# Kernel optimization log

Hardware: AMD Instinct MI355X
Metric: run time of the kernel (lower is better)

## Reference

```python
import jax, jax.numpy as jnp
import numpy as np

MUL = 16          # multiplicity of every irrep block
N = 131072        # number of nodes

# orthonormal traceless-symmetric 3x3 basis, divided by sqrt(5).
_s = 1.0 / np.sqrt(2.0)
_M = np.zeros((5, 3, 3), dtype=np.float32)
_M[0, 0, 1] = _M[0, 1, 0] = _s
_M[1, 0, 2] = _M[1, 2, 0] = _s
_M[2, 1, 2] = _M[2, 2, 1] = _s
_M[3, 0, 0] = _s; _M[3, 1, 1] = -_s
_M[4] = np.diag([-1.0, -1.0, 2.0]).astype(np.float32) / np.sqrt(6.0)
C112 = jnp.asarray(np.transpose(_M, (1, 2, 0)) / np.sqrt(5.0))  # (3,3,5)

# e3nn TensorProduct normalization: irrep_normalization='component'
# (alpha = 2l_out+1), path_normalization='element' (divide by sum of
# mul_u*mul_v over paths into the same output irrep). 0e output receives
# two paths -> 2*MUL^2; 1o and 2e each receive one path -> MUL^2.
A000 = float(np.sqrt(1.0 / (2.0 * MUL * MUL)))                    # 0e x 0e -> 0e (w3j = 1)
A110 = float(np.sqrt(1.0 / (2.0 * MUL * MUL)) / np.sqrt(3.0))     # 1o x 1o -> 0e (w3j = d_ij/sqrt(3))
A101 = float(np.sqrt(3.0 / (MUL * MUL)) / np.sqrt(3.0))           # 1o x 0e -> 1o (w3j = d_ik/sqrt(3))
A112 = float(np.sqrt(5.0 / (MUL * MUL)))                          # 1o x 1o -> 2e


def setup_inputs() -> dict:
    key = jax.random.key(0)
    ks = jax.random.split(key, 6)
    f = lambda k, s: jax.random.normal(k, s, dtype=jnp.float32)
    return {
        "node_feats": f(ks[0], (N, 4 * MUL)),
        "node_messages": f(ks[1], (N, 4 * MUL)),
        "w000": f(ks[2], (MUL, MUL, MUL)),
        "w101": f(ks[3], (MUL, MUL, MUL)),
        "w110": f(ks[4], (MUL, MUL, MUL)),
        "w112": f(ks[5], (MUL, MUL, MUL)),
    }


def _tensor_square(x, w000, w101, w110, w112):
    """e3nn o3.TensorSquare('16x0e+16x1o', '16x0e+16x1o+16x2e') with 'uvw' weighted paths."""
    n = x.shape[0]
    x0 = x[:, :MUL]                          # (n, u)     l=0 block
    x1 = x[:, MUL:].reshape(n, MUL, 3)       # (n, u, i)  l=1 block (mul-major)

    # --- 0e output ---
    out0 = A000 * jnp.einsum('uvw,nu,nv->nw', w000, x0, x0)
    out0 = out0 + A110 * jnp.einsum('uvw,nui,nvi->nw', w110, x1, x1)

    # --- 1o output ---
    out1 = A101 * jnp.einsum('uvw,nuk,nv->nwk', w101, x1, x0)

    # --- 2e output (staged to keep intermediates small) ---
    t1 = jnp.einsum('nvj,ijk->nvik', x1, C112)        # (n, v, i, 5)
    t = jnp.einsum('nui,nvik->nuvk', x1, t1)          # (n, u, v, 5)
    out2 = A112 * jnp.einsum('uvw,nuvk->nwk', w112, t)

    return jnp.concatenate(
        [out0, out1.reshape(n, 3 * MUL), out2.reshape(n, 5 * MUL)], axis=1
    )  # (n, 144)


def reference(node_feats, node_messages, w000, w101, w110, w112):
    # SimpleNodeBlock: sum all nodewise tensors, then tensor square.
    return _tensor_square(node_feats + node_messages, w000, w101, w110, w112)
```

## Files before the change

### kernel.cpp

```cpp
#include <hip/hip_runtime.h>

#define MUL 16
#define NPAIR 136
#define NTILE 25

typedef __bf16 bf16x8 __attribute__((ext_vector_type(8)));
typedef float  f32x4  __attribute__((ext_vector_type(4)));

__device__ __forceinline__ void uv_of(int p, int& u, int& v) {
    if (p >= NPAIR) { u = 0; v = 0; return; }
    int uu = 0, rem = p;
    while (rem >= MUL - uu) { rem -= MUL - uu; ++uu; }
    u = uu; v = uu + rem;
}

__global__ void prep_weights(const float* __restrict__ w000,
                             const float* __restrict__ w101,
                             const float* __restrict__ w110,
                             const float* __restrict__ w112,
                             __bf16* __restrict__ wt) {
    const int gid = blockIdx.x * 256 + threadIdx.x;
    if (gid >= NTILE * 64) return;
    const int T = gid >> 6, lane = gid & 63;
    const int q = lane >> 4, w = lane & 15;

    const float A000   = 0.044194173824159216f;
    const float A110   = 0.025515518153991442f;
    const float A101   = 0.0625f;
    const float A112C1 = 0.044194173824159216f;

    bf16x8 frag = {};
    if (T < 10) {
        const int c = T >> 1, b = T & 1;
#pragma unroll
        for (int i = 0; i < 4; ++i) {
            const int p = 32 * c + 8 * q + 4 * b + i;
            if (p < NPAIR) {
                int u, v; uv_of(p, u, v);
                const int uvw = (u * MUL + v) * MUL + w;
                const int vuw = (v * MUL + u) * MUL + w;
                float f000, f110;
                if (u == v) { f000 = A000 * w000[uvw]; f110 = A110 * w110[uvw]; }
                else        { f000 = A000 * (w000[uvw] + w000[vuw]);
                              f110 = A110 * (w110[uvw] + w110[vuw]); }
                frag[2 * i]     = (__bf16)f000;
                frag[2 * i + 1] = (__bf16)f110;
            }
        }
    } else if (T < 20) {
        const int c = (T - 10) >> 1, b = (T - 10) & 1;
#pragma unroll
        for (int i = 0; i < 4; ++i) {
            const int p = 32 * c + 8 * q + 4 * b + i;
            if (p < NPAIR) {
                int u, v; uv_of(p, u, v);
                const int uvw = (u * MUL + v) * MUL + w;
                const int vuw = (v * MUL + u) * MUL + w;
                frag[2 * i]     = (__bf16)(A101 * w101[uvw]);
                frag[2 * i + 1] = (__bf16)((u == v) ? 0.f : A101 * w101[vuw]);
            }
        }
    } else {
        const int c = T - 20;
#pragma unroll
        for (int e = 0; e < 8; ++e) {
            const int p = 32 * c + 8 * q + e;
            if (p < NPAIR) {
                int u, v; uv_of(p, u, v);
                const int uvw = (u * MUL + v) * MUL + w;
                const int vuw = (v * MUL + u) * MUL + w;
                const float f112 = (u == v) ? A112C1 * w112[uvw]
                                            : A112C1 * (w112[uvw] + w112[vuw]);
                frag[e] = (__bf16)f112;
            }
        }
    }
    ((bf16x8*)wt)[T * 64 + lane] = frag;
}

#define SQ3f  1.7320508075688772f
#define ISQ3f 0.5773502691896258f

template<int E>
__device__ __forceinline__ void pair_feats(int d, const float* __restrict__ xrow,
        bf16x8& fS, bf16x8& f0, bf16x8& f1, bf16x8& f2,
        bf16x8& t0, bf16x8& t1, bf16x8& t2, bf16x8& t3, bf16x8& t4) {
    constexpr int sh = (E & 1) * 16;
    const int u = (d >> sh) & 0xff;
    const int v = (d >> (sh + 8)) & 0xff;
    const float4 xu = *(const float4*)(xrow + 4 * u);
    const float4 xv = *(const float4*)(xrow + 4 * v);
    const float o00 = xu.y * xv.y, o01 = xu.y * xv.z, o02 = xu.y * xv.w;
    const float o10 = xu.z * xv.y, o11 = xu.z * xv.z, o12 = xu.z * xv.w;
    const float o20 = xu.w * xv.y, o21 = xu.w * xv.z, o22 = xu.w * xv.w;
    const float s1 = (o00 + o11) + o22;
    constexpr int s2 = (E & 3) * 2;
    fS[s2]     = (__bf16)(xu.x * xv.x);
    fS[s2 + 1] = (__bf16)s1;
    f0[s2]     = (__bf16)(xu.y * xv.x);  f0[s2 + 1] = (__bf16)(xv.y * xu.x);
    f1[s2]     = (__bf16)(xu.z * xv.x);  f1[s2 + 1] = (__bf16)(xv.z * xu.x);
    f2[s2]     = (__bf16)(xu.w * xv.x);  f2[s2 + 1] = (__bf16)(xv.w * xu.x);
    t0[E] = (__bf16)(o01 + o10);
    t1[E] = (__bf16)(o02 + o20);
    t2[E] = (__bf16)(o12 + o21);
    t3[E] = (__bf16)(o00 - o11);
    t4[E] = (__bf16)(SQ3f * o22 - ISQ3f * s1);
}

__launch_bounds__(256, 3)
__global__ void tsq_kernel(const float* __restrict__ feats,
                           const float* __restrict__ msgs,
                           const __bf16* __restrict__ wtiles,
                           float* __restrict__ out) {
    __shared__ __align__(16) float xq[64 * 68];
    __shared__ __align__(16) int   uvt[80];

    const int tid = threadIdx.x;
    const long long blockNode = (long long)blockIdx.x * 64;

    if (tid < 80) {
        int u0, v0, u1, v1;
        uv_of(2 * tid,     u0, v0);
        uv_of(2 * tid + 1, u1, v1);
        uvt[tid] = u0 | (v0 << 8) | (u1 << 16) | (v1 << 24);
    }

    {
        const float4* f4p = (const float4*)(feats + blockNode * 64);
        const float4* m4p = (const float4*)(msgs  + blockNode * 64);
#pragma unroll
        for (int r = 0; r < 4; ++r) {
            const int li = r * 256 + tid;
            const int nd = li >> 4, f4 = li & 15;
            const float4 a = f4p[li];
            const float4 b = m4p[li];
            const float vals[4] = {a.x + b.x, a.y + b.y, a.z + b.z, a.w + b.w};
#pragma unroll
            for (int jj = 0; jj < 4; ++jj) {
                const int f = 4 * f4 + jj;
                int dst;
                if (f < 16) dst = nd * 68 + 4 * f;
                else {
                    const int g = f - 16;
                    const int v3 = (g * 171) >> 9;
                    dst = nd * 68 + 4 * v3 + 1 + (g - 3 * v3);
                }
                xq[dst] = vals[jj];
            }
        }
    }
    __syncthreads();

    const int lane = tid & 63;
    const int wid  = tid >> 6;
    const int m = lane & 15, q = lane >> 4;
    const float* xrow = xq + (wid * 16 + m) * 68;
    const bf16x8* wb = (const bf16x8*)wtiles;

    f32x4 accS  = {0.f, 0.f, 0.f, 0.f};
    f32x4 accP0 = {0.f, 0.f, 0.f, 0.f};
    f32x4 accP1 = {0.f, 0.f, 0.f, 0.f};
    f32x4 accP2 = {0.f, 0.f, 0.f, 0.f};
    f32x4 accT0 = {0.f, 0.f, 0.f, 0.f};
    f32x4 accT1 = {0.f, 0.f, 0.f, 0.f};
    f32x4 accT2 = {0.f, 0.f, 0.f, 0.f};
    f32x4 accT3 = {0.f, 0.f, 0.f, 0.f};
    f32x4 accT4 = {0.f, 0.f, 0.f, 0.f};

#pragma unroll
    for (int c = 0; c < 5; ++c) {
        const int4 uvd = *(const int4*)((const char*)uvt + 64 * c + 16 * q);
        bf16x8 t0 = {}, t1 = {}, t2 = {}, t3 = {}, t4 = {};
        {
            const bf16x8 bS = wb[(2 * c) * 64 + lane];
            const bf16x8 bP = wb[(10 + 2 * c) * 64 + lane];
            bf16x8 fS, f0, f1, f2;
            pair_feats<0>(uvd.x, xrow, fS, f0, f1, f2, t0, t1, t2, t3, t4);
            pair_feats<1>(uvd.x, xrow, fS, f0, f1, f2, t0, t1, t2, t3, t4);
            pair_feats<2>(uvd.y, xrow, fS, f0, f1, f2, t0, t1, t2, t3, t4);
            pair_feats<3>(uvd.y, xrow, fS, f0, f1, f2, t0, t1, t2, t3, t4);
            accS  = __builtin_amdgcn_mfma_f32_16x16x32_bf16(fS, bS, accS,  0, 0, 0);
            accP0 = __builtin_amdgcn_mfma_f32_16x16x32_bf16(f0, bP, accP0, 0, 0, 0);
            accP1 = __builtin_amdgcn_mfma_f32_16x16x32_bf16(f1, bP, accP1, 0, 0, 0);
            accP2 = __builtin_amdgcn_mfma_f32_16x16x32_bf16(f2, bP, accP2, 0, 0, 0);
        }
        {
            const bf16x8 bS = wb[(2 * c + 1) * 64 + lane];
            const bf16x8 bP = wb[(11 + 2 * c) * 64 + lane];
            bf16x8 fS, f0, f1, f2;
            pair_feats<4>(uvd.z, xrow, fS, f0, f1, f2, t0, t1, t2, t3, t4);
            pair_feats<5>(uvd.z, xrow, fS, f0, f1, f2, t0, t1, t2, t3, t4);
            pair_feats<6>(uvd.w, xrow, fS, f0, f1, f2, t0, t1, t2, t3, t4);
            pair_feats<7>(uvd.w, xrow, fS, f0, f1, f2, t0, t1, t2, t3, t4);
            accS  = __builtin_amdgcn_mfma_f32_16x16x32_bf16(fS, bS, accS,  0, 0, 0);
            accP0 = __builtin_amdgcn_mfma_f32_16x16x32_bf16(f0, bP, accP0, 0, 0, 0);
            accP1 = __builtin_amdgcn_mfma_f32_16x16x32_bf16(f1, bP, accP1, 0, 0, 0);
            accP2 = __builtin_amdgcn_mfma_f32_16x16x32_bf16(f2, bP, accP2, 0, 0, 0);
        }
        const bf16x8 bT = wb[(20 + c) * 64 + lane];
        accT0 = __builtin_amdgcn_mfma_f32_16x16x32_bf16(t0, bT, accT0, 0, 0, 0);
        accT1 = __builtin_amdgcn_mfma_f32_16x16x32_bf16(t1, bT, accT1, 0, 0, 0);
        accT2 = __builtin_amdgcn_mfma_f32_16x16x32_bf16(t2, bT, accT2, 0, 0, 0);
        accT3 = __builtin_amdgcn_mfma_f32_16x16x32_bf16(t3, bT, accT3, 0, 0, 0);
        accT4 = __builtin_amdgcn_mfma_f32_16x16x32_bf16(t4, bT, accT4, 0, 0, 0);
    }

#pragma unroll
    for (int r = 0; r < 4; ++r) {
        float* ob = out + (blockNode + wid * 16 + q * 4 + r) * 144;
        ob[m]              = accS[r];
        ob[16 + 3 * m + 0] = accP0[r];
        ob[16 + 3 * m + 1] = accP1[r];
        ob[16 + 3 * m + 2] = accP2[r];
        ob[64 + 5 * m + 0] = accT0[r];
        ob[64 + 5 * m + 1] = accT1[r];
        ob[64 + 5 * m + 2] = accT2[r];
        ob[64 + 5 * m + 3] = accT3[r];
        ob[64 + 5 * m + 4] = accT4[r];
    }
}

extern "C" void kernel_launch(void* const* d_in, const int* in_sizes, int n_in,
                              void* d_out, int out_size, void* d_ws, size_t ws_size,
                              hipStream_t stream) {
    const float* feats = (const float*)d_in[0];
    const float* msgs  = (const float*)d_in[1];
    const float* w000  = (const float*)d_in[2];
    const float* w101  = (const float*)d_in[3];
    const float* w110  = (const float*)d_in[4];
    const float* w112  = (const float*)d_in[5];
    __bf16* wt = (__bf16*)d_ws;
    float* out = (float*)d_out;

    const int n = in_sizes[0] / (4 * MUL);

    prep_weights<<<(NTILE * 64 + 255) / 256, 256, 0, stream>>>(w000, w101, w110, w112, wt);
    tsq_kernel<<<n / 64, 256, 0, stream>>>(feats, msgs, wt, out);
}
```

Before: 161.9 us.

## Regroup pair enumeration by u-rows, shrink blocks to one wave, pack FP32 products

The flat 136-pair enumeration is replaced by groups that share a common u, so each lane loads x_u once per chunk and walks consecutive v values. This removes the packed uv lookup table, but the padding grows from 5 to 6 chunks (30 weight tiles) and adds more MFMA work on zero entries. Blocks shrink from 256 threads over 64 nodes to 64 threads over 16 nodes, which cuts LDS per block and gives finer scheduling. The outer products are rewritten as 2-wide float vector multiplies so the compiler can emit packed FP32 instructions.

```diff
diff --git a/kernel.cpp b/kernel.cpp
--- a/kernel.cpp
+++ b/kernel.cpp
@@ -1,17 +1,16 @@
 #include <hip/hip_runtime.h>
 
 #define MUL 16
-#define NPAIR 136
-#define NTILE 25
+#define NTILE 30
+#define NCHUNK 6
 
 typedef __bf16 bf16x8 __attribute__((ext_vector_type(8)));
+typedef float  f32x2  __attribute__((ext_vector_type(2)));
 typedef float  f32x4  __attribute__((ext_vector_type(4)));
 
-__device__ __forceinline__ void uv_of(int p, int& u, int& v) {
-    if (p >= NPAIR) { u = 0; v = 0; return; }
-    int uu = 0, rem = p;
-    while (rem >= MUL - uu) { rem -= MUL - uu; ++uu; }
-    u = uu; v = uu + rem;
+__device__ __forceinline__ void group_uvs(int g, int& u, int& vs) {
+    if (g < 16) { u = g >> 1; vs = u + ((g & 1) << 3); }
+    else        { u = g - 8;  vs = u; }
 }
 
 __global__ void prep_weights(const float* __restrict__ w000,
@@ -30,13 +29,13 @@
     const float A112C1 = 0.044194173824159216f;
 
     bf16x8 frag = {};
-    if (T < 10) {
-        const int c = T >> 1, b = T & 1;
+    if (T < 12) {
+        const int c = T >> 1, h = T & 1;
+        int u, vs; group_uvs(4 * c + q, u, vs);
 #pragma unroll
         for (int i = 0; i < 4; ++i) {
-            const int p = 32 * c + 8 * q + 4 * b + i;
-            if (p < NPAIR) {
-                int u, v; uv_of(p, u, v);
+            const int v = vs + 4 * h + i;
+            if (v < 16) {
                 const int uvw = (u * MUL + v) * MUL + w;
                 const int vuw = (v * MUL + u) * MUL + w;
                 float f000, f110;
@@ -47,13 +46,13 @@
                 frag[2 * i + 1] = (__bf16)f110;
             }
         }
-    } else if (T < 20) {
-        const int c = (T - 10) >> 1, b = (T - 10) & 1;
+    } else if (T < 24) {
+        const int c = (T - 12) >> 1, h = (T - 12) & 1;
+        int u, vs; group_uvs(4 * c + q, u, vs);
 #pragma unroll
         for (int i = 0; i < 4; ++i) {
-            const int p = 32 * c + 8 * q + 4 * b + i;
-            if (p < NPAIR) {
-                int u, v; uv_of(p, u, v);
+            const int v = vs + 4 * h + i;
+            if (v < 16) {
                 const int uvw = (u * MUL + v) * MUL + w;
                 const int vuw = (v * MUL + u) * MUL + w;
                 frag[2 * i]     = (__bf16)(A101 * w101[uvw]);
@@ -61,12 +60,12 @@
             }
         }
     } else {
-        const int c = T - 20;
+        const int c = T - 24;
+        int u, vs; group_uvs(4 * c + q, u, vs);
 #pragma unroll
         for (int e = 0; e < 8; ++e) {
-            const int p = 32 * c + 8 * q + e;
-            if (p < NPAIR) {
-                int u, v; uv_of(p, u, v);
+            const int v = vs + e;
+            if (v < 16) {
                 const int uvw = (u * MUL + v) * MUL + w;
                 const int vuw = (v * MUL + u) * MUL + w;
                 const float f112 = (u == v) ? A112C1 * w112[uvw]
@@ -81,56 +80,63 @@
 #define SQ3f  1.7320508075688772f
 #define ISQ3f 0.5773502691896258f
 
-template<int E>
-__device__ __forceinline__ void pair_feats(int d, const float* __restrict__ xrow,
+template<int J>
+__device__ __forceinline__ void do_pair(int vs, const float* __restrict__ xrow,
+        const float4 xu,
         bf16x8& fS, bf16x8& f0, bf16x8& f1, bf16x8& f2,
         bf16x8& t0, bf16x8& t1, bf16x8& t2, bf16x8& t3, bf16x8& t4) {
-    constexpr int sh = (E & 1) * 16;
-    const int u = (d >> sh) & 0xff;
-    const int v = (d >> (sh + 8)) & 0xff;
-    const float4 xu = *(const float4*)(xrow + 4 * u);
+    int v = vs + J;
+    v = v < 15 ? v : 15;
     const float4 xv = *(const float4*)(xrow + 4 * v);
-    const float o00 = xu.y * xv.y, o01 = xu.y * xv.z, o02 = xu.y * xv.w;
-    const float o10 = xu.z * xv.y, o11 = xu.z * xv.z, o12 = xu.z * xv.w;
-    const float o20 = xu.w * xv.y, o21 = xu.w * xv.z, o22 = xu.w * xv.w;
+
+    const f32x2 U01 = {xu.x, xu.y};
+    const f32x2 U23 = {xu.z, xu.w};
+    const f32x2 U10 = {xu.y, xu.x};
+    const f32x2 V01 = {xv.x, xv.y};
+    const f32x2 V23 = {xv.z, xv.w};
+    const f32x2 V10 = {xv.y, xv.x};
+    const f32x2 V32 = {xv.w, xv.z};
+
+    const f32x2 P1 = U01 * V01;
+    const f32x2 P2 = U23 * V23;
+    const f32x2 P3 = U01 * V23;
+    const f32x2 P4 = U23 * V01;
+    const f32x2 P5 = U01 * V32;
+    const f32x2 P6 = U23 * V10;
+    const f32x2 P7 = U23 * V32;
+    const f32x2 P8 = U10 * V01;
+
+    const float o00 = P1[1], o11 = P2[0], o22 = P2[1];
     const float s1 = (o00 + o11) + o22;
-    constexpr int s2 = (E & 3) * 2;
-    fS[s2]     = (__bf16)(xu.x * xv.x);
-    fS[s2 + 1] = (__bf16)s1;
-    f0[s2]     = (__bf16)(xu.y * xv.x);  f0[s2 + 1] = (__bf16)(xv.y * xu.x);
-    f1[s2]     = (__bf16)(xu.z * xv.x);  f1[s2 + 1] = (__bf16)(xv.z * xu.x);
-    f2[s2]     = (__bf16)(xu.w * xv.x);  f2[s2 + 1] = (__bf16)(xv.w * xu.x);
-    t0[E] = (__bf16)(o01 + o10);
-    t1[E] = (__bf16)(o02 + o20);
-    t2[E] = (__bf16)(o12 + o21);
-    t3[E] = (__bf16)(o00 - o11);
-    t4[E] = (__bf16)(SQ3f * o22 - ISQ3f * s1);
-}
-
-__launch_bounds__(256, 3)
+
+    constexpr int s2 = (J & 3) * 2;
+    fS[s2]     = (__bf16)P1[0];  fS[s2 + 1] = (__bf16)s1;
+    f0[s2]     = (__bf16)P8[0];  f0[s2 + 1] = (__bf16)P8[1];
+    f1[s2]     = (__bf16)P4[0];  f1[s2 + 1] = (__bf16)P3[0];
+    f2[s2]     = (__bf16)P6[1];  f2[s2 + 1] = (__bf16)P5[0];
+    t0[J] = (__bf16)(P5[1] + P6[0]);
+    t1[J] = (__bf16)(P3[1] + P4[1]);
+    t2[J] = (__bf16)(P7[0] + P7[1]);
+    t3[J] = (__bf16)(o00 - o11);
+    t4[J] = (__bf16)(SQ3f * o22 - ISQ3f * s1);
+}
+
+__launch_bounds__(64, 4)
 __global__ void tsq_kernel(const float* __restrict__ feats,
                            const float* __restrict__ msgs,
                            const __bf16* __restrict__ wtiles,
                            float* __restrict__ out) {
-    __shared__ __align__(16) float xq[64 * 68];
-    __shared__ __align__(16) int   uvt[80];
+    __shared__ __align__(16) float xq[16 * 68];
 
     const int tid = threadIdx.x;
-    const long long blockNode = (long long)blockIdx.x * 64;
-
-    if (tid < 80) {
-        int u0, v0, u1, v1;
-        uv_of(2 * tid,     u0, v0);
-        uv_of(2 * tid + 1, u1, v1);
-        uvt[tid] = u0 | (v0 << 8) | (u1 << 16) | (v1 << 24);
-    }
+    const long long blockNode = (long long)blockIdx.x * 16;
 
     {
         const float4* f4p = (const float4*)(feats + blockNode * 64);
         const float4* m4p = (const float4*)(msgs  + blockNode * 64);
 #pragma unroll
         for (int r = 0; r < 4; ++r) {
-            const int li = r * 256 + tid;
+            const int li = r * 64 + tid;
             const int nd = li >> 4, f4 = li & 15;
             const float4 a = f4p[li];
             const float4 b = m4p[li];
@@ -151,10 +157,9 @@
     }
     __syncthreads();
 
-    const int lane = tid & 63;
-    const int wid  = tid >> 6;
+    const int lane = tid;
     const int m = lane & 15, q = lane >> 4;
-    const float* xrow = xq + (wid * 16 + m) * 68;
+    const float* xrow = xq + m * 68;
     const bf16x8* wb = (const bf16x8*)wtiles;
 
     f32x4 accS  = {0.f, 0.f, 0.f, 0.f};
@@ -168,36 +173,41 @@
     f32x4 accT4 = {0.f, 0.f, 0.f, 0.f};
 
 #pragma unroll
-    for (int c = 0; c < 5; ++c) {
-        const int4 uvd = *(const int4*)((const char*)uvt + 64 * c + 16 * q);
+    for (int c = 0; c < NCHUNK; ++c) {
+        int u, vs;
+        if (c < 4) { u = 2 * c + (q >> 1); vs = u + ((q & 1) << 3); }
+        else       { u = 4 * c - 8 + q;    vs = u; }
+        const float4 xu = *(const float4*)(xrow + 4 * u);
+
+        const bf16x8 bS0 = wb[(2 * c) * 64 + lane];
+        const bf16x8 bS1 = wb[(2 * c + 1) * 64 + lane];
+        const bf16x8 bP0 = wb[(12 + 2 * c) * 64 + lane];
+        const bf16x8 bP1 = wb[(13 + 2 * c) * 64 + lane];
+        const bf16x8 bT  = wb[(24 + c) * 64 + lane];
+
         bf16x8 t0 = {}, t1 = {}, t2 = {}, t3 = {}, t4 = {};
         {
-            const bf16x8 bS = wb[(2 * c) * 64 + lane];
-            const bf16x8 bP = wb[(10 + 2 * c) * 64 + lane];
             bf16x8 fS, f0, f1, f2;
-            pair_feats<0>(uvd.x, xrow, fS, f0, f1, f2, t0, t1, t2, t3, t4);
-            pair_feats<1>(uvd.x, xrow, fS, f0, f1, f2, t0, t1, t2, t3, t4);
-            pair_feats<2>(uvd.y, xrow, fS, f0, f1, f2, t0, t1, t2, t3, t4);
-            pair_feats<3>(uvd.y, xrow, fS, f0, f1, f2, t0, t1, t2, t3, t4);
-            accS  = __builtin_amdgcn_mfma_f32_16x16x32_bf16(fS, bS, accS,  0, 0, 0);
-            accP0 = __builtin_amdgcn_mfma_f32_16x16x32_bf16(f0, bP, accP0, 0, 0, 0);
-            accP1 = __builtin_amdgcn_mfma_f32_16x16x32_bf16(f1, bP, accP1, 0, 0, 0);
-            accP2 = __builtin_amdgcn_mfma_f32_16x16x32_bf16(f2, bP, accP2, 0, 0, 0);
+            do_pair<0>(vs, xrow, xu, fS, f0, f1, f2, t0, t1, t2, t3, t4);
+            do_pair<1>(vs, xrow, xu, fS, f0, f1, f2, t0, t1, t2, t3, t4);
+            do_pair<2>(vs, xrow, xu, fS, f0, f1, f2, t0, t1, t2, t3, t4);
+            do_pair<3>(vs, xrow, xu, fS, f0, f1, f2, t0, t1, t2, t3, t4);
+            accS  = __builtin_amdgcn_mfma_f32_16x16x32_bf16(fS, bS0, accS,  0, 0, 0);
+            accP0 = __builtin_amdgcn_mfma_f32_16x16x32_bf16(f0, bP0, accP0, 0, 0, 0);
+            accP1 = __builtin_amdgcn_mfma_f32_16x16x32_bf16(f1, bP0, accP1, 0, 0, 0);
+            accP2 = __builtin_amdgcn_mfma_f32_16x16x32_bf16(f2, bP0, accP2, 0, 0, 0);
         }
         {
-            const bf16x8 bS = wb[(2 * c + 1) * 64 + lane];
-            const bf16x8 bP = wb[(11 + 2 * c) * 64 + lane];
             bf16x8 fS, f0, f1, f2;
-            pair_feats<4>(uvd.z, xrow, fS, f0, f1, f2, t0, t1, t2, t3, t4);
-            pair_feats<5>(uvd.z, xrow, fS, f0, f1, f2, t0, t1, t2, t3, t4);
-            pair_feats<6>(uvd.w, xrow, fS, f0, f1, f2, t0, t1, t2, t3, t4);
-            pair_feats<7>(uvd.w, xrow, fS, f0, f1, f2, t0, t1, t2, t3, t4);
-            accS  = __builtin_amdgcn_mfma_f32_16x16x32_bf16(fS, bS, accS,  0, 0, 0);
-            accP0 = __builtin_amdgcn_mfma_f32_16x16x32_bf16(f0, bP, accP0, 0, 0, 0);
-            accP1 = __builtin_amdgcn_mfma_f32_16x16x32_bf16(f1, bP, accP1, 0, 0, 0);
-            accP2 = __builtin_amdgcn_mfma_f32_16x16x32_bf16(f2, bP, accP2, 0, 0, 0);
-        }
-        const bf16x8 bT = wb[(20 + c) * 64 + lane];
+            do_pair<4>(vs, xrow, xu, fS, f0, f1, f2, t0, t1, t2, t3, t4);
+            do_pair<5>(vs, xrow, xu, fS, f0, f1, f2, t0, t1, t2, t3, t4);
+            do_pair<6>(vs, xrow, xu, fS, f0, f1, f2, t0, t1, t2, t3, t4);
+            do_pair<7>(vs, xrow, xu, fS, f0, f1, f2, t0, t1, t2, t3, t4);
+            accS  = __builtin_amdgcn_mfma_f32_16x16x32_bf16(fS, bS1, accS,  0, 0, 0);
+            accP0 = __builtin_amdgcn_mfma_f32_16x16x32_bf16(f0, bP1, accP0, 0, 0, 0);
+            accP1 = __builtin_amdgcn_mfma_f32_16x16x32_bf16(f1, bP1, accP1, 0, 0, 0);
+            accP2 = __builtin_amdgcn_mfma_f32_16x16x32_bf16(f2, bP1, accP2, 0, 0, 0);
+        }
         accT0 = __builtin_amdgcn_mfma_f32_16x16x32_bf16(t0, bT, accT0, 0, 0, 0);
         accT1 = __builtin_amdgcn_mfma_f32_16x16x32_bf16(t1, bT, accT1, 0, 0, 0);
         accT2 = __builtin_amdgcn_mfma_f32_16x16x32_bf16(t2, bT, accT2, 0, 0, 0);
@@ -207,7 +217,7 @@
 
 #pragma unroll
     for (int r = 0; r < 4; ++r) {
-        float* ob = out + (blockNode + wid * 16 + q * 4 + r) * 144;
+        float* ob = out + (blockNode + q * 4 + r) * 144;
         ob[m]              = accS[r];
         ob[16 + 3 * m + 0] = accP0[r];
         ob[16 + 3 * m + 1] = accP1[r];
@@ -235,5 +245,5 @@
     const int n = in_sizes[0] / (4 * MUL);
 
     prep_weights<<<(NTILE * 64 + 255) / 256, 256, 0, stream>>>(w000, w101, w110, w112, wt);
-    tsq_kernel<<<n / 64, 256, 0, stream>>>(feats, msgs, wt, out);
-}
+    tsq_kernel<<<n / 16, 64, 0, stream>>>(feats, msgs, wt, out);
+}
```

Result: slower. 179.0 us (+10.5%).
